# Optimization experiments

Measured on AMD Instinct MI355X. Metric: run time of the kernel, lower is better.

Reference implementation:

```python
import jax, jax.numpy as jnp
import numpy as np

EPS = 1e-8  # torch F.cosine_similarity eps


def setup_inputs() -> dict:
    key = jax.random.key(0)
    k1, k2 = jax.random.split(key)
    z = jax.random.normal(k1, (32768, 2048), dtype=jnp.float32)
    expert_keys = jax.random.normal(k2, (64, 2048), dtype=jnp.float32)
    return {"z": z, "expert_keys": expert_keys}


def reference(z, expert_keys):
    # cosine similarity: (z . ek) / max(||z||*||ek||, eps)  -> [N, E]
    dots = jnp.einsum("nd,ed->ne", z, expert_keys)
    z_norm = jnp.linalg.norm(z, axis=-1)            # [N]
    e_norm = jnp.linalg.norm(expert_keys, axis=-1)  # [E]
    similarity = dots / jnp.maximum(z_norm[:, None] * e_norm[None, :], EPS)
    # softmax over experts, then weighted combination of expert keys -> [N, D]
    weighted_expert = jax.nn.softmax(similarity, axis=-1) @ expert_keys
    return similarity, weighted_expert
```

## Files before the change

kernel.cpp:

```cpp
#include <hip/hip_runtime.h>
#include <hip/hip_bf16.h>

typedef __attribute__((ext_vector_type(4))) float f32x4;
typedef __attribute__((ext_vector_type(8))) short bf16x8;

#define NROWS 32768
#define DIM   2048
#define NEXP  64
#define BKF   128
#define NCH   (DIM / BKF)

__device__ __forceinline__ short f2bf(float f) {
    __hip_bfloat16 h = __float2bfloat16(f);
    short s;
    __builtin_memcpy(&s, &h, 2);
    return s;
}

__device__ __forceinline__ void async16(const void* g, void* l) {
    __builtin_amdgcn_global_load_lds(
        (const __attribute__((address_space(1))) unsigned int*)g,
        (__attribute__((address_space(3))) unsigned int*)l, 16, 0, 0);
}

__global__ __launch_bounds__(256) void prep_experts(
    const float* __restrict__ ek,
    short* __restrict__ ekbf,
    short* __restrict__ ekT,
    float* __restrict__ enorm)
{
    const int e = blockIdx.x;
    const int t = threadIdx.x;
    const float* row = ek + e * DIM;
    float ss = 0.f;
#pragma unroll
    for (int i = 0; i < 2; ++i) {
        const int c4 = t + i * 256;
        const float4 v = ((const float4*)row)[c4];
        ss += v.x * v.x + v.y * v.y + v.z * v.z + v.w * v.w;
        short4 b;
        b.x = f2bf(v.x); b.y = f2bf(v.y); b.z = f2bf(v.z); b.w = f2bf(v.w);
        *(short4*)(ekbf + e * DIM + c4 * 4) = b;
        const int d = c4 * 4;
        ekT[(d + 0) * NEXP + e] = b.x;
        ekT[(d + 1) * NEXP + e] = b.y;
        ekT[(d + 2) * NEXP + e] = b.z;
        ekT[(d + 3) * NEXP + e] = b.w;
    }
#pragma unroll
    for (int s = 1; s < 64; s <<= 1) ss += __shfl_xor(ss, s);
    __shared__ float red[4];
    if ((t & 63) == 0) red[t >> 6] = ss;
    __syncthreads();
    if (t == 0) enorm[e] = sqrtf(red[0] + red[1] + red[2] + red[3]);
}

__global__ __launch_bounds__(256) void sim_kernel(
    const float* __restrict__ z,
    const short* __restrict__ ekbf,
    const float* __restrict__ enorm,
    float* __restrict__ out_sim)
{
    const int tid = threadIdx.x;
    const int w   = tid >> 6;
    const int l   = tid & 63;
    const int lr  = l & 15;
    const int lg  = l >> 4;
    const int base = blockIdx.x * 32;

    __shared__ __align__(16) float zbuf[2][32][BKF];
    __shared__ __align__(16) short ebuf[2][64][BKF];

    f32x4 acc[2];
    acc[0] = f32x4{0.f, 0.f, 0.f, 0.f};
    acc[1] = f32x4{0.f, 0.f, 0.f, 0.f};
    float sqa[2] = {0.f, 0.f}, sqb[2] = {0.f, 0.f};

    auto STAGE = [&](int c_) {
        const int b_ = c_ & 1;
#pragma unroll
        for (int i = 0; i < 4; ++i) {
            const int r0 = w * 8 + i * 2;
            const int zr = r0 + (l >> 5);
            async16(z + (size_t)(base + zr) * DIM + c_ * BKF
                      + (((l & 31) ^ (zr & 7)) << 2),
                    &zbuf[b_][r0][0]);
        }
#pragma unroll
        for (int i = 0; i < 4; ++i) {
            const int r0 = w * 16 + i * 4;
            const int er = r0 + (l >> 4);
            async16(ekbf + (size_t)er * DIM + c_ * BKF
                         + (((l & 15) ^ (er & 7)) << 3),
                    &ebuf[b_][r0][0]);
        }
    };

    STAGE(0); STAGE(1);

    for (int c = 0; c < NCH; ++c) {
        if (c < NCH - 1) asm volatile("s_waitcnt vmcnt(8)" ::: "memory");
        else             asm volatile("s_waitcnt vmcnt(0)" ::: "memory");
        __builtin_amdgcn_s_barrier();
        __builtin_amdgcn_sched_barrier(0);
        const int b = c & 1;

#pragma unroll
        for (int kk = 0; kk < BKF / 32; ++kk) {
            const int eu = ((kk * 4 + lg) ^ (lr & 7)) << 4;
            const bf16x8 bf =
                *(const bf16x8*)((const char*)&ebuf[b][w * 16 + lr][0] + eu);
#pragma unroll
            for (int mt = 0; mt < 2; ++mt) {
                const int zr = mt * 16 + lr;
                const int u0 = ((kk * 8 + lg * 2)     ^ (lr & 7)) << 4;
                const int u1 = ((kk * 8 + lg * 2 + 1) ^ (lr & 7)) << 4;
                const float4 a0 = *(const float4*)((const char*)&zbuf[b][zr][0] + u0);
                const float4 a1 = *(const float4*)((const char*)&zbuf[b][zr][0] + u1);
                sqa[mt] = fmaf(a0.x, a0.x, sqa[mt]); sqb[mt] = fmaf(a0.y, a0.y, sqb[mt]);
                sqa[mt] = fmaf(a0.z, a0.z, sqa[mt]); sqb[mt] = fmaf(a0.w, a0.w, sqb[mt]);
                sqa[mt] = fmaf(a1.x, a1.x, sqa[mt]); sqb[mt] = fmaf(a1.y, a1.y, sqb[mt]);
                sqa[mt] = fmaf(a1.z, a1.z, sqa[mt]); sqb[mt] = fmaf(a1.w, a1.w, sqb[mt]);
                bf16x8 af;
                af[0] = f2bf(a0.x); af[1] = f2bf(a0.y); af[2] = f2bf(a0.z); af[3] = f2bf(a0.w);
                af[4] = f2bf(a1.x); af[5] = f2bf(a1.y); af[6] = f2bf(a1.z); af[7] = f2bf(a1.w);
                acc[mt] = __builtin_amdgcn_mfma_f32_16x16x32_bf16(af, bf, acc[mt], 0, 0, 0);
            }
        }
        __builtin_amdgcn_s_barrier();
        if (c + 2 < NCH) STAGE(c + 2);
    }

    const float en = enorm[w * 16 + lr];
#pragma unroll
    for (int mt = 0; mt < 2; ++mt) {
        float ss = sqa[mt] + sqb[mt];
        ss += __shfl_xor(ss, 16);
        ss += __shfl_xor(ss, 32);
        const float zn = sqrtf(ss);
#pragma unroll
        for (int j = 0; j < 4; ++j) {
            const float znj = __shfl(zn, lg * 4 + j);
            out_sim[(size_t)(base + mt * 16 + lg * 4 + j) * NEXP + w * 16 + lr]
                = acc[mt][j] / fmaxf(znj * en, 1e-8f);
        }
    }
}

__global__ __launch_bounds__(256) void moe_kernel(
    const float* __restrict__ sim,
    const short* __restrict__ ekT,
    float* __restrict__ out_wei)
{
    const int tid = threadIdx.x;
    const int w   = tid >> 6;
    const int l   = tid & 63;
    const int lr  = l & 15;
    const int lg  = l >> 4;
    const int base = blockIdx.x * 32;
    const int col0 = blockIdx.y * 1024 + w * 256;

    __shared__ __align__(16) short WL[32][64];
    __shared__ __align__(16) float tbuf[4][32][68];

    {
        const int r  = tid >> 3;
        const int cc = tid & 7;
        const float* sp = sim + (size_t)(base + r) * NEXP + cc * 8;
        const float4 v0 = *(const float4*)sp;
        const float4 v1 = *(const float4*)(sp + 4);
        float va[8] = {v0.x, v0.y, v0.z, v0.w, v1.x, v1.y, v1.z, v1.w};
        float m = va[0];
#pragma unroll
        for (int i = 1; i < 8; ++i) m = fmaxf(m, va[i]);
        m = fmaxf(m, __shfl_xor(m, 1));
        m = fmaxf(m, __shfl_xor(m, 2));
        m = fmaxf(m, __shfl_xor(m, 4));
        float sum = 0.f;
#pragma unroll
        for (int i = 0; i < 8; ++i) { va[i] = __expf(va[i] - m); sum += va[i]; }
        sum += __shfl_xor(sum, 1);
        sum += __shfl_xor(sum, 2);
        sum += __shfl_xor(sum, 4);
        const float inv = 1.0f / sum;
        bf16x8 wv;
#pragma unroll
        for (int i = 0; i < 8; ++i) wv[i] = f2bf(va[i] * inv);
        *(bf16x8*)&WL[r][(cc ^ (r & 7)) * 8] = wv;
    }
    __syncthreads();

    bf16x8 afr[2][2];
#pragma unroll
    for (int mt = 0; mt < 2; ++mt)
#pragma unroll
        for (int ks = 0; ks < 2; ++ks) {
            const int row = mt * 16 + lr;
            const int u   = (ks * 4 + lg) ^ (row & 7);
            afr[mt][ks] = *(const bf16x8*)&WL[row][u * 8];
        }

#pragma unroll 1
    for (int g = 0; g < 4; ++g) {
        f32x4 oacc[4][2];
#pragma unroll
        for (int nt2 = 0; nt2 < 4; ++nt2) {
            const int d0 = col0 + g * 64 + nt2 * 16;
            const short* bp = ekT + (size_t)(d0 + lr) * NEXP + lg * 8;
            const bf16x8 b0 = *(const bf16x8*)bp;
            const bf16x8 b1 = *(const bf16x8*)(bp + 32);
#pragma unroll
            for (int mt = 0; mt < 2; ++mt) {
                f32x4 o = f32x4{0.f, 0.f, 0.f, 0.f};
                o = __builtin_amdgcn_mfma_f32_16x16x32_bf16(afr[mt][0], b0, o, 0, 0, 0);
                o = __builtin_amdgcn_mfma_f32_16x16x32_bf16(afr[mt][1], b1, o, 0, 0, 0);
                oacc[nt2][mt] = o;
            }
        }
#pragma unroll
        for (int nt2 = 0; nt2 < 4; ++nt2)
#pragma unroll
            for (int mt = 0; mt < 2; ++mt)
#pragma unroll
                for (int j = 0; j < 4; ++j)
                    tbuf[w][mt * 16 + lg * 4 + j][nt2 * 16 + lr] = oacc[nt2][mt][j];
#pragma unroll
        for (int i = 0; i < 8; ++i) {
            const int row  = (l >> 4) + i * 4;
            const int unit = l & 15;
            const float4 t = *(const float4*)&tbuf[w][row][unit * 4];
            *(float4*)&out_wei[(size_t)(base + row) * DIM + col0 + g * 64 + unit * 4] = t;
        }
    }
}

extern "C" void kernel_launch(void* const* d_in, const int* in_sizes, int n_in,
                              void* d_out, int out_size, void* d_ws, size_t ws_size,
                              hipStream_t stream) {
    const float* z  = (const float*)d_in[0];
    const float* ek = (const float*)d_in[1];
    float* out_sim = (float*)d_out;
    float* out_wei = out_sim + (size_t)NROWS * NEXP;

    short* ekbf  = (short*)d_ws;
    short* ekT   = ekbf + NEXP * DIM;
    float* enorm = (float*)(ekT + DIM * NEXP);

    prep_experts<<<NEXP, 256, 0, stream>>>(ek, ekbf, ekT, enorm);
    sim_kernel<<<NROWS / 32, 256, 0, stream>>>(z, ekbf, enorm, out_sim);
    moe_kernel<<<dim3(NROWS / 32, 2), 256, 0, stream>>>(out_sim, ekT, out_wei);
}
```

Measured before the change: 147.5 us.

## Fuse similarity and softmax-combine kernels into one block-per-row-tile kernel

After: 130.8 us, median of 2. 1.13x faster.

```diff
diff --git a/kernel.cpp b/kernel.cpp
--- a/kernel.cpp
+++ b/kernel.cpp
@@ -55,11 +55,13 @@
     if (t == 0) enorm[e] = sqrtf(red[0] + red[1] + red[2] + red[3]);
 }
 
-__global__ __launch_bounds__(256) void sim_kernel(
+__global__ __launch_bounds__(256) void fused_kernel(
     const float* __restrict__ z,
     const short* __restrict__ ekbf,
+    const short* __restrict__ ekT,
     const float* __restrict__ enorm,
-    float* __restrict__ out_sim)
+    float* __restrict__ out_sim,
+    float* __restrict__ out_wei)
 {
     const int tid = threadIdx.x;
     const int w   = tid >> 6;
@@ -68,8 +70,14 @@
     const int lg  = l >> 4;
     const int base = blockIdx.x * 32;
 
-    __shared__ __align__(16) float zbuf[2][32][BKF];
+    union SmemU {
+        float zbuf[2][32][BKF];
+        float tbuf[4][32][68];
+    };
+    __shared__ __align__(16) SmemU U;
     __shared__ __align__(16) short ebuf[2][64][BKF];
+    __shared__ __align__(16) float simL[32][64];
+    __shared__ __align__(16) short WL[32][64];
 
     f32x4 acc[2];
     acc[0] = f32x4{0.f, 0.f, 0.f, 0.f};
@@ -84,7 +92,7 @@
             const int zr = r0 + (l >> 5);
             async16(z + (size_t)(base + zr) * DIM + c_ * BKF
                       + (((l & 31) ^ (zr & 7)) << 2),
-                    &zbuf[b_][r0][0]);
+                    &U.zbuf[b_][r0][0]);
         }
 #pragma unroll
         for (int i = 0; i < 4; ++i) {
@@ -115,8 +123,8 @@
                 const int zr = mt * 16 + lr;
                 const int u0 = ((kk * 8 + lg * 2)     ^ (lr & 7)) << 4;
                 const int u1 = ((kk * 8 + lg * 2 + 1) ^ (lr & 7)) << 4;
-                const float4 a0 = *(const float4*)((const char*)&zbuf[b][zr][0] + u0);
-                const float4 a1 = *(const float4*)((const char*)&zbuf[b][zr][0] + u1);
+                const float4 a0 = *(const float4*)((const char*)&U.zbuf[b][zr][0] + u0);
+                const float4 a1 = *(const float4*)((const char*)&U.zbuf[b][zr][0] + u1);
                 sqa[mt] = fmaf(a0.x, a0.x, sqa[mt]); sqb[mt] = fmaf(a0.y, a0.y, sqb[mt]);
                 sqa[mt] = fmaf(a0.z, a0.z, sqa[mt]); sqb[mt] = fmaf(a0.w, a0.w, sqb[mt]);
                 sqa[mt] = fmaf(a1.x, a1.x, sqa[mt]); sqb[mt] = fmaf(a1.y, a1.y, sqb[mt]);
@@ -141,35 +149,20 @@
 #pragma unroll
         for (int j = 0; j < 4; ++j) {
             const float znj = __shfl(zn, lg * 4 + j);
-            out_sim[(size_t)(base + mt * 16 + lg * 4 + j) * NEXP + w * 16 + lr]
-                = acc[mt][j] / fmaxf(znj * en, 1e-8f);
-        }
-    }
-}
-
-__global__ __launch_bounds__(256) void moe_kernel(
-    const float* __restrict__ sim,
-    const short* __restrict__ ekT,
-    float* __restrict__ out_wei)
-{
-    const int tid = threadIdx.x;
-    const int w   = tid >> 6;
-    const int l   = tid & 63;
-    const int lr  = l & 15;
-    const int lg  = l >> 4;
-    const int base = blockIdx.x * 32;
-    const int col0 = blockIdx.y * 1024 + w * 256;
-
-    __shared__ __align__(16) short WL[32][64];
-    __shared__ __align__(16) float tbuf[4][32][68];
+            const float sv = acc[mt][j] / fmaxf(znj * en, 1e-8f);
+            out_sim[(size_t)(base + mt * 16 + lg * 4 + j) * NEXP + w * 16 + lr] = sv;
+            simL[mt * 16 + lg * 4 + j][w * 16 + lr] = sv;
+        }
+    }
+    __syncthreads();
 
     {
         const int r  = tid >> 3;
         const int cc = tid & 7;
-        const float* sp = sim + (size_t)(base + r) * NEXP + cc * 8;
-        const float4 v0 = *(const float4*)sp;
-        const float4 v1 = *(const float4*)(sp + 4);
-        float va[8] = {v0.x, v0.y, v0.z, v0.w, v1.x, v1.y, v1.z, v1.w};
+        const float* sp = &simL[r][cc * 8];
+        const f32x4 v0 = *(const f32x4*)sp;
+        const f32x4 v1 = *(const f32x4*)(sp + 4);
+        float va[8] = {v0[0], v0[1], v0[2], v0[3], v1[0], v1[1], v1[2], v1[3]};
         float m = va[0];
 #pragma unroll
         for (int i = 1; i < 8; ++i) m = fmaxf(m, va[i]);
@@ -201,11 +194,11 @@
         }
 
 #pragma unroll 1
-    for (int g = 0; g < 4; ++g) {
+    for (int g = 0; g < 8; ++g) {
         f32x4 oacc[4][2];
 #pragma unroll
         for (int nt2 = 0; nt2 < 4; ++nt2) {
-            const int d0 = col0 + g * 64 + nt2 * 16;
+            const int d0 = w * 512 + g * 64 + nt2 * 16;
             const short* bp = ekT + (size_t)(d0 + lr) * NEXP + lg * 8;
             const bf16x8 b0 = *(const bf16x8*)bp;
             const bf16x8 b1 = *(const bf16x8*)(bp + 32);
@@ -223,13 +216,13 @@
             for (int mt = 0; mt < 2; ++mt)
 #pragma unroll
                 for (int j = 0; j < 4; ++j)
-                    tbuf[w][mt * 16 + lg * 4 + j][nt2 * 16 + lr] = oacc[nt2][mt][j];
+                    U.tbuf[w][mt * 16 + lg * 4 + j][nt2 * 16 + lr] = oacc[nt2][mt][j];
 #pragma unroll
         for (int i = 0; i < 8; ++i) {
             const int row  = (l >> 4) + i * 4;
             const int unit = l & 15;
-            const float4 t = *(const float4*)&tbuf[w][row][unit * 4];
-            *(float4*)&out_wei[(size_t)(base + row) * DIM + col0 + g * 64 + unit * 4] = t;
+            const float4 t = *(const float4*)&U.tbuf[w][row][unit * 4];
+            *(float4*)&out_wei[(size_t)(base + row) * DIM + w * 512 + g * 64 + unit * 4] = t;
         }
     }
 }
@@ -247,6 +240,5 @@
     float* enorm = (float*)(ekT + DIM * NEXP);
 
     prep_experts<<<NEXP, 256, 0, stream>>>(ek, ekbf, ekT, enorm);
-    sim_kernel<<<NROWS / 32, 256, 0, stream>>>(z, ekbf, enorm, out_sim);
-    moe_kernel<<<dim3(NROWS / 32, 2), 256, 0, stream>>>(out_sim, ekT, out_wei);
-}
+    fused_kernel<<<NROWS / 32, 256, 0, stream>>>(z, ekbf, ekT, enorm, out_sim, out_wei);
+}
```
